# Optimization experiments

Hardware: AMD Instinct MI355X
Metric: run time of the kernel (lower is better)

The kernel has to match this reference:

```python
import jax, jax.numpy as jnp
import numpy as np

B, L = 8, 1024
VOCAB, D_ENC, D_MAIN = 260, 128, 256
N_ENC, N_MAIN, N_DEC, N_HEADS = 3, 6, 3, 4
N_RATIO = 6.0  # 1/target_ratio
NEG = jnp.float32(-1e9)


def setup_inputs() -> dict:
    key = jax.random.key(0)
    kc = iter(jax.random.split(key, 40))
    def nrm(shape, std):
        return jax.random.normal(next(kc), shape, jnp.float32) * std
    inp = {'byte_ids': jax.random.randint(next(kc), (B, L), 0, VOCAB)}
    inp['embed'] = nrm((VOCAB, D_ENC), D_ENC ** -0.5)
    eye = jnp.eye(D_ENC, dtype=jnp.float32)
    inp['wq'] = eye + nrm((D_ENC, D_ENC), 0.02)  # init is identity in the torch module
    inp['wk'] = eye + nrm((D_ENC, D_ENC), 0.02)
    inp['proj_up'] = nrm((D_MAIN, D_ENC), D_ENC ** -0.5)
    inp['proj_down'] = nrm((D_ENC, D_MAIN), 1e-3)
    inp['norm_w'] = jnp.ones((D_ENC,), jnp.float32)
    inp['norm_b'] = jnp.zeros((D_ENC,), jnp.float32)
    for pre, n, d in [('enc', N_ENC, D_ENC), ('main', N_MAIN, D_MAIN), ('dec', N_DEC, D_ENC)]:
        inp[pre + '_ln1_w'] = jnp.ones((n, d), jnp.float32)
        inp[pre + '_ln1_b'] = jnp.zeros((n, d), jnp.float32)
        inp[pre + '_qkv'] = nrm((n, 3 * d, d), d ** -0.5)   # MHA in_proj (3D, D)
        inp[pre + '_wo'] = nrm((n, d, d), d ** -0.5)        # MHA out_proj
        inp[pre + '_ln2_w'] = jnp.ones((n, d), jnp.float32)
        inp[pre + '_ln2_b'] = jnp.zeros((n, d), jnp.float32)
        inp[pre + '_w1'] = nrm((n, 2 * d, d), d ** -0.5)    # mlp_mult = 2
        inp[pre + '_w2'] = nrm((n, d, 2 * d), (2 * d) ** -0.5)
    return inp


def _ln(x, w, b):
    mu = jnp.mean(x, axis=-1, keepdims=True)
    var = jnp.mean((x - mu) ** 2, axis=-1, keepdims=True)
    return (x - mu) * jax.lax.rsqrt(var + 1e-5) * w + b


def _mha(x, wqkv, wo, bias):
    Bb, S, D = x.shape
    dh = D // N_HEADS
    q, k, v = jnp.split(x @ wqkv.T, 3, axis=-1)
    q = q.reshape(Bb, S, N_HEADS, dh)
    k = k.reshape(Bb, S, N_HEADS, dh)
    v = v.reshape(Bb, S, N_HEADS, dh)
    scores = jnp.einsum('bqhd,bkhd->bhqk', q, k) * (dh ** -0.5) + bias
    attn = jax.nn.softmax(scores, axis=-1)
    out = jnp.einsum('bhqk,bkhd->bqhd', attn, v).reshape(Bb, S, D)
    return out @ wo.T


def _block(x, stack, i, bias):
    ln1w, ln1b, qkv, wo, ln2w, ln2b, w1, w2 = (a[i] for a in stack)
    x = x + _mha(_ln(x, ln1w, ln1b), qkv, wo, bias)
    h = _ln(x, ln2w, ln2b)
    return x + jax.nn.gelu(h @ w1.T, approximate=False) @ w2.T


def _downsample(x, b_hard):
    # scatter boundary tokens to the front of a padded (B, S, D) buffer
    Bb, S, D = x.shape
    idx = jnp.cumsum(b_hard, axis=1).astype(jnp.int32) - 1
    dest = jnp.where(b_hard > 0.5, idx, S)  # S is out-of-range -> dropped
    def sc(xb, db):
        return jnp.zeros((S, D), xb.dtype).at[db].set(xb, mode='drop')
    out = jax.vmap(sc)(x, dest)
    counts = jnp.sum(b_hard, axis=1).astype(jnp.int32)
    mask = jnp.arange(S)[None, :] < counts[:, None]
    return out, mask


def _forward(byte_ids, embed, wq, wk,
             enc_ln1_w, enc_ln1_b, enc_qkv, enc_wo, enc_ln2_w, enc_ln2_b, enc_w1, enc_w2,
             proj_up,
             main_ln1_w, main_ln1_b, main_qkv, main_wo, main_ln2_w, main_ln2_b, main_w1, main_w2,
             proj_down,
             dec_ln1_w, dec_ln1_b, dec_qkv, dec_wo, dec_ln2_w, dec_ln2_b, dec_w1, dec_w2,
             norm_w, norm_b):
    causal = jnp.where(jnp.triu(jnp.ones((L, L), bool), 1), NEG, jnp.float32(0.0))[None, None]
    x = embed[byte_ids]  # (B, L, D_ENC)
    enc_p = (enc_ln1_w, enc_ln1_b, enc_qkv, enc_wo, enc_ln2_w, enc_ln2_b, enc_w1, enc_w2)
    for i in range(N_ENC):
        x = _block(x, enc_p, i, causal)

    # --- dynamic chunking (routing + ratio loss) ---
    def l2n(t):
        return t / jnp.maximum(jnp.linalg.norm(t, axis=-1, keepdims=True), 1e-12)
    q = l2n(x @ wq.T)
    k = l2n(x @ wk.T)
    k_prev = jnp.pad(k[:, :-1], ((0, 0), (1, 0), (0, 0)))
    cos = jnp.sum(q * k_prev, axis=-1)
    p = jnp.clip(0.5 * (1.0 - cos), 0.0, 1.0)
    p = jnp.concatenate([jnp.ones_like(p[:, :1]), p[:, 1:]], axis=1)
    b_hard = (p >= 0.5).astype(jnp.float32)
    N = N_RATIO
    F_act = jnp.mean(b_hard)
    G_act = jnp.mean(p)
    ratio_loss = N / (N - 1.0) * ((N - 1.0) * F_act * G_act + (1.0 - F_act) * (1.0 - G_act))
    compressed, comp_mask = _downsample(x, b_hard)
    p_comp = _downsample(p[..., None], b_hard)[0][..., 0]

    # --- main stack on compressed sequence (padded to L, masked) ---
    z = compressed @ proj_up.T
    main_bias = causal + jnp.where(comp_mask, jnp.float32(0.0), NEG)[:, None, None, :]
    main_p = (main_ln1_w, main_ln1_b, main_qkv, main_wo, main_ln2_w, main_ln2_b, main_w1, main_w2)
    for i in range(N_MAIN):
        z = _block(z, main_p, i, main_bias)
    z = z @ proj_down.T  # (B, L, D_ENC)

    # --- chunk-level EMA (parallel linear-recurrence scan) + gather + STE ---
    p_c = jnp.clip(p_comp, 1e-4, 1.0 - 1e-4)
    a = (1.0 - p_c).at[:, 0].set(0.0)[..., None]          # z_bar[0] = z[0]
    bv = (p_c[..., None] * z).at[:, :1].set(z[:, :1])
    def comb(lhs, rhs):
        al, bl = lhs
        ar, br = rhs
        return (al * ar, ar * bl + br)
    z_bar = jax.lax.associative_scan(comb, (a, bv), axis=1)[1]
    chunk_idx = jnp.clip(jnp.cumsum(b_hard, axis=1).astype(jnp.int32) - 1, 0, None)
    z_up = jnp.take_along_axis(z_bar, jnp.broadcast_to(chunk_idx[:, :, None], z_bar.shape), axis=1)
    c = b_hard * p + (1.0 - b_hard) * (1.0 - p)
    c_ste = c + jax.lax.stop_gradient(1.0 - c)
    x = x + c_ste[..., None] * z_up

    dec_p = (dec_ln1_w, dec_ln1_b, dec_qkv, dec_wo, dec_ln2_w, dec_ln2_b, dec_w1, dec_w2)
    for i in range(N_DEC):
        x = _block(x, dec_p, i, causal)
    x = _ln(x, norm_w, norm_b)
    logits = x @ embed.T  # tied head
    return logits, ratio_loss


def reference(byte_ids, embed, wq, wk,
              enc_ln1_w, enc_ln1_b, enc_qkv, enc_wo, enc_ln2_w, enc_ln2_b, enc_w1, enc_w2,
              proj_up,
              main_ln1_w, main_ln1_b, main_qkv, main_wo, main_ln2_w, main_ln2_b, main_w1, main_w2,
              proj_down,
              dec_ln1_w, dec_ln1_b, dec_qkv, dec_wo, dec_ln2_w, dec_ln2_b, dec_w1, dec_w2,
              norm_w, norm_b):
    return _forward(byte_ids, embed, wq, wk,
                    enc_ln1_w, enc_ln1_b, enc_qkv, enc_wo, enc_ln2_w, enc_ln2_b, enc_w1, enc_w2,
                    proj_up,
                    main_ln1_w, main_ln1_b, main_qkv, main_wo, main_ln2_w, main_ln2_b, main_w1, main_w2,
                    proj_down,
                    dec_ln1_w, dec_ln1_b, dec_qkv, dec_wo, dec_ln2_w, dec_ln2_b, dec_w1, dec_w2,
                    norm_w, norm_b)
```

## Files before the change

### kernel.cpp

```cpp
#include <hip/hip_runtime.h>
#include <hip/hip_bf16.h>

#define B_ 8
#define L_ 1024
#define BL (B_*L_)
#define DENC 128
#define DMAIN 256
#define VOCAB 260
#define NHEADS 4

typedef __hip_bfloat16 bf16;
typedef _Float16 f16;
typedef f16 half8 __attribute__((ext_vector_type(8)));
typedef float f32x4 __attribute__((ext_vector_type(4)));

__global__ __launch_bounds__(64) void k_detect(const void* __restrict__ emb, int* __restrict__ flag){
    int lane = threadIdx.x;
    const unsigned short* u = (const unsigned short*)emb;
    int bad = 0;
    #pragma unroll
    for (int j = 0; j < 4; j++){
        unsigned short h = u[lane + 64*j];
        bf16 t = *(const bf16*)&h;
        float v = __bfloat162float(t);
        if (!(fabsf(v) < 1e4f)) bad++;
    }
    #pragma unroll
    for (int o = 32; o >= 1; o >>= 1) bad += __shfl_xor(bad, o);
    if (lane == 0) flag[0] = (bad == 0) ? 1 : 0;
}

struct CvtArgs {
    const void* src[31];
    unsigned offs[32];
};
__global__ void k_cvt_all(CvtArgs a, float* __restrict__ dst, int total, const int* __restrict__ flag){
    int isbf = flag[0];
    for (int i = blockIdx.x*256 + threadIdx.x; i < total; i += gridDim.x*256){
        int lo = 0, hi = 30;
        while (lo < hi){ int mid = (lo+hi+1)>>1; if (a.offs[mid] <= (unsigned)i) lo = mid; else hi = mid-1; }
        int j = i - (int)a.offs[lo];
        dst[i] = isbf ? __bfloat162float(((const bf16*)a.src[lo])[j])
                      : ((const float*)a.src[lo])[j];
    }
}

__global__ void k_embed(const int* __restrict__ ids, const float* __restrict__ emb, float* __restrict__ x){
    int i = blockIdx.x*256 + threadIdx.x;
    int row = i >> 7, d = i & 127;
    x[i] = emb[ids[row]*DENC + d];
}

template<int D>
__global__ __launch_bounds__(256) void k_ln(const float* __restrict__ x, const float* __restrict__ w,
                                            const float* __restrict__ b, float* __restrict__ y){
    int row = blockIdx.x*4 + (threadIdx.x >> 6);
    int lane = threadIdx.x & 63;
    const float* xr = x + (size_t)row*D;
    float v[D/64];
    float s = 0.f;
    #pragma unroll
    for (int j=0;j<D/64;j++){ v[j] = xr[lane + j*64]; s += v[j]; }
    #pragma unroll
    for (int o=32;o>=1;o>>=1) s += __shfl_xor(s,o);
    float mu = s / (float)D;
    float s2 = 0.f;
    #pragma unroll
    for (int j=0;j<D/64;j++){ float dd = v[j]-mu; s2 += dd*dd; }
    #pragma unroll
    for (int o=32;o>=1;o>>=1) s2 += __shfl_xor(s2,o);
    float inv = rsqrtf(s2/(float)D + 1e-5f);
    float* yr = y + (size_t)row*D;
    #pragma unroll
    for (int j=0;j<D/64;j++){
        int d = lane + j*64;
        yr[d] = (v[j]-mu)*inv*w[d] + b[d];
    }
}

#define GBM 64
#define GBN 64
#define GBK 32
__global__ __launch_bounds__(256) void k_gemm2(const float* __restrict__ A, const float* __restrict__ Wq,
        const float* __restrict__ Wk, float* __restrict__ Cq, float* __restrict__ Ck, int K)
{
    __shared__ float As[GBK][GBM+4];
    __shared__ float Ws[GBK][GBN+4];
    int tid = threadIdx.x;
    int bm = blockIdx.y * GBM;
    int bn = blockIdx.x * GBN;
    int tx = tid & 15, ty = tid >> 4;
    float acc[4][4] = {};
    for (int k0 = 0; k0 < K; k0 += GBK){
        #pragma unroll
        for (int i = tid; i < GBM*GBK; i += 256){
            int m = i >> 5, kk = i & 31;
            As[kk][m] = A[(size_t)(bm+m)*K + k0 + kk];
        }
        #pragma unroll
        for (int i = tid; i < GBN*GBK; i += 256){
            int n = i >> 5, kk = i & 31;
            int gn = bn + n;
            const float* W = (gn < 128) ? Wq : Wk;
            int wr = gn & 127;
            Ws[kk][n] = W[(size_t)wr*K + k0 + kk];
        }
        __syncthreads();
        #pragma unroll
        for (int kk = 0; kk < GBK; kk++){
            float a0[4], w0[4];
            *(float4*)a0 = *(const float4*)&As[kk][ty*4];
            *(float4*)w0 = *(const float4*)&Ws[kk][tx*4];
            #pragma unroll
            for (int i=0;i<4;i++)
                #pragma unroll
                for (int j=0;j<4;j++) acc[i][j] += a0[i]*w0[j];
        }
        __syncthreads();
    }
    #pragma unroll
    for (int i=0;i<4;i++){
        int m = bm + ty*4 + i;
        #pragma unroll
        for (int j=0;j<4;j++){
            int n = bn + tx*4 + j;
            float* C = (n < 128) ? Cq : Ck;
            C[(size_t)m*128 + (n & 127)] = acc[i][j];
        }
    }
}

__global__ __launch_bounds__(256) void k_mgemm(const float* __restrict__ A, const float* __restrict__ W,
        const float* __restrict__ R, float* __restrict__ C, void* __restrict__ OutRaw,
        const int* __restrict__ flag, int M, int N, int K, int mode,
        f16* __restrict__ Qd, f16* __restrict__ Kd, f16* __restrict__ Vd,
        int dShift, int dhShift)
{
    __shared__ half8 As[4][64];
    __shared__ half8 Ws[4][64];
    int tid = threadIdx.x;
    int wave = tid >> 6, lane = tid & 63;
    int wr = wave >> 1, wc = wave & 1;
    int quad = lane >> 4, l15 = lane & 15;
    int bm = blockIdx.y * 64;
    int bn = blockIdx.x * 64;

    f32x4 acc[2][2] = {};

    int srow = tid >> 2;
    int sc8  = tid & 3;
    const float* ap0 = A + (size_t)(bm + srow)*K + sc8*8;
    int gn = bn + srow;
    const float* wp0 = W + (size_t)gn*K + sc8*8;
    bool wok = (gn < N);

    for (int k0 = 0; k0 < K; k0 += 32){
        __syncthreads();
        {
            const float* ap = ap0 + k0;
            float4 u0 = *(const float4*)(ap);
            float4 u1 = *(const float4*)(ap+4);
            half8 h0;
            h0[0]=(f16)u0.x; h0[1]=(f16)u0.y; h0[2]=(f16)u0.z; h0[3]=(f16)u0.w;
            h0[4]=(f16)u1.x; h0[5]=(f16)u1.y; h0[6]=(f16)u1.z; h0[7]=(f16)u1.w;
            As[sc8][srow] = h0;
            half8 g0 = (half8)(f16)0.f;
            if (wok){
                const float* wp = wp0 + k0;
                float4 v0 = *(const float4*)(wp);
                float4 v1 = *(const float4*)(wp+4);
                g0[0]=(f16)v0.x; g0[1]=(f16)v0.y; g0[2]=(f16)v0.z; g0[3]=(f16)v0.w;
                g0[4]=(f16)v1.x; g0[5]=(f16)v1.y; g0[6]=(f16)v1.z; g0[7]=(f16)v1.w;
            }
            Ws[sc8][srow] = g0;
        }
        __syncthreads();

        half8 af[2], wf[2];
        #pragma unroll
        for (int i=0;i<2;i++) af[i] = As[quad][wr*32 + i*16 + l15];
        #pragma unroll
        for (int j=0;j<2;j++) wf[j] = Ws[quad][wc*32 + j*16 + l15];
        #pragma unroll
        for (int i=0;i<2;i++)
            #pragma unroll
            for (int j=0;j<2;j++)
                acc[i][j] = __builtin_amdgcn_mfma_f32_16x16x32_f16(af[i], wf[j], acc[i][j], 0, 0, 0);
    }

    #pragma unroll
    for (int j=0;j<2;j++){
        int n = bn + wc*32 + j*16 + l15;
        if (n >= N) continue;
        #pragma unroll
        for (int i=0;i<2;i++){
            #pragma unroll
            for (int r=0;r<4;r++){
                int m = bm + wr*32 + i*16 + quad*4 + r;
                float v = acc[i][j][r];
                if (mode == 5){
                    int which = n >> dShift;
                    int rem = n & ((1<<dShift)-1);
                    int hh = rem >> dhShift;
                    int dd = rem & ((1<<dhShift)-1);
                    int bb = m >> 10, tt = m & 1023;
                    int Hn = 1 << (dShift - dhShift);
                    f16* dst = (which==0) ? Qd : ((which==1) ? Kd : Vd);
                    if (which == 2)
                        dst[((((size_t)bb*Hn + hh) << dhShift) + dd)*L_ + tt] = (f16)v;
                    else
                        dst[((((size_t)bb*Hn + hh)*L_ + tt) << dhShift) + dd] = (f16)v;
                    continue;
                }
                size_t off = (size_t)m*N + n;
                if (mode == 1) v += R[off];
                else if (mode == 2) v = 0.5f*v*(1.0f + erff(v*0.70710678118654752f));
                if (mode == 3){
                    if (flag[0]) ((bf16*)OutRaw)[off] = __float2bfloat16(v);
                    else         ((float*)OutRaw)[off] = v;
                } else C[off] = v;
            }
        }
    }
}

template<int DH>
__global__ __launch_bounds__(256) void k_mflash(const f16* __restrict__ Qh, const f16* __restrict__ Kh,
        const f16* __restrict__ Vt, float* __restrict__ out, const int* __restrict__ counts,
        float scale)
{
    constexpr int BQ = 64, BK = 64;
    constexpr int RS = DH + 8;
    constexpr int PS = BK + 8;
    __shared__ f16 sQ[BQ*RS];
    __shared__ f16 sK[BK*RS];
    __shared__ f16 sVt[DH*PS];
    __shared__ f16 sP[BQ*PS];

    int x = blockIdx.x, b = x >> 2, h = x & 3;
    int yy = blockIdx.y;
    int qt = (yy < 8) ? yy : 23 - yy;
    int q0 = qt * BQ;
    int tid = threadIdx.x;
    int wv = tid >> 6, lane = tid & 63;
    int quad = lane >> 4, l15 = lane & 15;

    const f16* Qb = Qh + (size_t)x*L_*DH;
    const f16* Kb = Kh + (size_t)x*L_*DH;
    const f16* Vb = Vt + (size_t)x*DH*L_;
    int kcap = counts ? counts[b] : L_;
    int klen = min(kcap, q0 + BQ);

    for (int i = tid; i < BQ*DH/8; i += 256){
        int r = (8*i)/DH, c = (8*i)%DH;
        *(half8*)&sQ[r*RS + c] = *(const half8*)&Qb[(size_t)(q0+r)*DH + c];
    }

    float m[4], l[4];
    #pragma unroll
    for (int r=0;r<4;r++){ m[r] = -1e30f; l[r] = 0.f; }
    f32x4 accO[DH/16] = {};

    for (int k0 = 0; k0 < klen; k0 += BK){
        __syncthreads();
        for (int i = tid; i < BK*DH/8; i += 256){
            int r = (8*i)/DH, c = (8*i)%DH;
            *(half8*)&sK[r*RS + c] = *(const half8*)&Kb[(size_t)(k0+r)*DH + c];
        }
        for (int i = tid; i < DH*BK/8; i += 256){
            int r = (8*i)/BK, c = (8*i)%BK;
            *(half8*)&sVt[r*PS + c] = *(const half8*)&Vb[(size_t)r*L_ + k0 + c];
        }
        __syncthreads();

        half8 af[DH/32];
        #pragma unroll
        for (int ds=0; ds<DH/32; ds++)
            af[ds] = *(const half8*)&sQ[(16*wv + l15)*RS + quad*8 + 32*ds];
        f32x4 accS[4] = {};
        #pragma unroll
        for (int t=0;t<4;t++){
            #pragma unroll
            for (int ds=0; ds<DH/32; ds++){
                half8 bf = *(const half8*)&sK[(16*t + l15)*RS + quad*8 + 32*ds];
                accS[t] = __builtin_amdgcn_mfma_f32_16x16x32_f16(af[ds], bf, accS[t], 0, 0, 0);
            }
        }

        #pragma unroll
        for (int r=0;r<4;r++){
            int qrow = q0 + 16*wv + quad*4 + r;
            float sv[4];
            #pragma unroll
            for (int t=0;t<4;t++){
                float v = accS[t][r]*scale;
                int kp = k0 + 16*t + l15;
                if (kp > qrow || kp >= kcap) v = -1e30f;
                sv[t] = v;
            }
            float rm = fmaxf(fmaxf(sv[0],sv[1]), fmaxf(sv[2],sv[3]));
            rm = fmaxf(rm, __shfl_xor(rm, 1));
            rm = fmaxf(rm, __shfl_xor(rm, 2));
            rm = fmaxf(rm, __shfl_xor(rm, 4));
            rm = fmaxf(rm, __shfl_xor(rm, 8));
            float mn = fmaxf(m[r], rm);
            float al = __expf(m[r] - mn);
            float p0 = __expf(sv[0]-mn), p1 = __expf(sv[1]-mn);
            float p2 = __expf(sv[2]-mn), p3 = __expf(sv[3]-mn);
            float rs = p0+p1+p2+p3;
            rs += __shfl_xor(rs, 1);
            rs += __shfl_xor(rs, 2);
            rs += __shfl_xor(rs, 4);
            rs += __shfl_xor(rs, 8);
            l[r] = l[r]*al + rs;
            m[r] = mn;
            #pragma unroll
            for (int dt=0; dt<DH/16; dt++) accO[dt][r] *= al;
            int prow = 16*wv + quad*4 + r;
            sP[prow*PS + 16*0 + l15] = (f16)p0;
            sP[prow*PS + 16*1 + l15] = (f16)p1;
            sP[prow*PS + 16*2 + l15] = (f16)p2;
            sP[prow*PS + 16*3 + l15] = (f16)p3;
        }

        half8 pf[2];
        #pragma unroll
        for (int ks=0; ks<2; ks++)
            pf[ks] = *(const half8*)&sP[(16*wv + l15)*PS + quad*8 + 32*ks];
        #pragma unroll
        for (int dt=0; dt<DH/16; dt++){
            #pragma unroll
            for (int ks=0; ks<2; ks++){
                half8 bv = *(const half8*)&sVt[(16*dt + l15)*PS + quad*8 + 32*ks];
                accO[dt] = __builtin_amdgcn_mfma_f32_16x16x32_f16(pf[ks], bv, accO[dt], 0, 0, 0);
            }
        }
    }

    #pragma unroll
    for (int r=0;r<4;r++){
        float inv = 1.0f / l[r];
        int qrow = q0 + 16*wv + quad*4 + r;
        #pragma unroll
        for (int dt=0; dt<DH/16; dt++){
            int d = 16*dt + l15;
            out[((size_t)b*L_ + qrow)*(NHEADS*DH) + h*DH + d] = accO[dt][r]*inv;
        }
    }
}

__global__ __launch_bounds__(64) void k_router(const float* __restrict__ Q, const float* __restrict__ Kr,
        float* __restrict__ p, float* __restrict__ bh)
{
    int idx = blockIdx.x;
    int t = idx & (L_-1);
    int lane = threadIdx.x;
    float pv;
    if (t == 0){ pv = 1.0f; }
    else {
        const float* qr = Q  + (size_t)idx*DENC;
        const float* kr = Kr + (size_t)(idx-1)*DENC;
        float qq=0.f, kk=0.f, qk=0.f;
        #pragma unroll
        for (int j=0;j<2;j++){
            float qv = qr[lane + j*64], kv = kr[lane + j*64];
            qq += qv*qv; kk += kv*kv; qk += qv*kv;
        }
        #pragma unroll
        for (int o=32;o>=1;o>>=1){ qq += __shfl_xor(qq,o); kk += __shfl_xor(kk,o); qk += __shfl_xor(qk,o); }
        float cosv = qk / (fmaxf(sqrtf(qq),1e-12f)*fmaxf(sqrtf(kk),1e-12f));
        pv = 0.5f*(1.0f - cosv);
        pv = fminf(fmaxf(pv, 0.0f), 1.0f);
    }
    if (lane == 0){ p[idx] = pv; bh[idx] = (pv >= 0.5f) ? 1.0f : 0.0f; }
}

__global__ __launch_bounds__(64) void k_seq(const float* __restrict__ bh, int* __restrict__ cidx,
                      int* __restrict__ dest, int* __restrict__ counts){
    int b = blockIdx.x;
    int lane = threadIdx.x;
    int base = b*L_ + lane*16;
    int h[16];
    int cnt = 0;
    #pragma unroll
    for (int j=0;j<16;j++){ h[j] = bh[base+j] > 0.5f; cnt += h[j]; }
    int inc = cnt;
    #pragma unroll
    for (int o=1;o<64;o<<=1){ int nb = __shfl_up(inc, o); if (lane >= o) inc += nb; }
    int run = inc - cnt;
    #pragma unroll
    for (int j=0;j<16;j++){
        run += h[j];
        int ci = run - 1; if (ci < 0) ci = 0;
        cidx[base+j] = ci;
        dest[base+j] = h[j] ? (run-1) : L_;
    }
    if (lane == 63) counts[b] = inc;
}

__global__ void k_zeroinit(float* __restrict__ comp, float* __restrict__ pcomp, float* __restrict__ acc){
    int i = blockIdx.x*256 + threadIdx.x;
    comp[i] = 0.f;
    if (i < BL) pcomp[i] = 0.f;
    if (i < 8) acc[i] = 0.f;
}

__global__ void k_scatter(const float* __restrict__ x, const float* __restrict__ p,
        const int* __restrict__ dest, const float* __restrict__ bh,
        float* __restrict__ comp, float* __restrict__ pcomp)
{
    int i = blockIdx.x;
    int d = threadIdx.x;
    int b = i >> 10;
    if (bh[i] > 0.5f){
        int ds = dest[i];
        comp[((size_t)b*L_ + ds)*DENC + d] = x[(size_t)i*DENC + d];
        if (d == 0) pcomp[b*L_ + ds] = p[i];
    }
}

__global__ __launch_bounds__(256) void k_reduce(const float* __restrict__ p, const float* __restrict__ bh,
                                                float* __restrict__ acc){
    __shared__ float sp[256], sb[256];
    int tid = threadIdx.x;
    float s1=0.f, s2=0.f;
    for (int i = blockIdx.x*256 + tid; i < BL; i += gridDim.x*256){ s1 += p[i]; s2 += bh[i]; }
    sp[tid]=s1; sb[tid]=s2; __syncthreads();
    for (int o=128;o>=1;o>>=1){ if (tid<o){ sp[tid]+=sp[tid+o]; sb[tid]+=sb[tid+o]; } __syncthreads(); }
    if (tid==0){ atomicAdd(&acc[0], sp[0]); atomicAdd(&acc[1], sb[0]); }
}

__global__ __launch_bounds__(256) void k_ema2(const float* __restrict__ z, const float* __restrict__ pcomp,
                                              float* __restrict__ zbar){
    __shared__ float sp[L_];
    int blk = blockIdx.x;
    int b = blk >> 5;
    int tid = threadIdx.x, wv = tid >> 6, lane = tid & 63;
    int d = ((blk & 31) << 2) + wv;
    for (int i = tid; i < L_; i += 256){
        float pc = pcomp[b*L_ + i];
        sp[i] = fminf(fmaxf(pc, 1e-4f), 1.0f - 1e-4f);
    }
    __syncthreads();
    const float* zb = z + ((size_t)b*L_)*DENC + d;
    int t0 = lane*16;
    float zv[16];
    #pragma unroll
    for (int i=0;i<16;i++) zv[i] = zb[(size_t)(t0+i)*DENC];
    float A = 1.f, Bv = 0.f;
    #pragma unroll
    for (int i=0;i<16;i++){
        int t = t0 + i;
        float pc = sp[t];
        float a  = (t==0) ? 0.f : (1.f - pc);
        float bb = (t==0) ? zv[i] : pc*zv[i];
        A = a*A;
        Bv = a*Bv + bb;
    }
    #pragma unroll
    for (int off=1; off<64; off<<=1){
        float Ap = __shfl_up(A, off);
        float Bp = __shfl_up(Bv, off);
        if (lane >= off){ Bv = A*Bp + Bv; A = A*Ap; }
    }
    float sin_ = __shfl_up(Bv, 1);
    if (lane == 0) sin_ = 0.f;
    float s = sin_;
    float* ob = zbar + ((size_t)b*L_)*DENC + d;
    #pragma unroll
    for (int i=0;i<16;i++){
        int t = t0 + i;
        float pc = sp[t];
        float a  = (t==0) ? 0.f : (1.f - pc);
        float bb = (t==0) ? zv[i] : pc*zv[i];
        s = a*s + bb;
        ob[(size_t)t*DENC] = s;
    }
}

__global__ void k_combine(float* __restrict__ x, const float* __restrict__ zbar, const int* __restrict__ cidx){
    int i = blockIdx.x*256 + threadIdx.x;
    int row = i >> 7, d = i & 127;
    int b = row >> 10;
    int ci = cidx[row];
    x[i] += zbar[((size_t)b*L_ + ci)*DENC + d];
}

__global__ void k_loss(const float* __restrict__ acc, void* __restrict__ out, const int* __restrict__ flag){
    float G = acc[0] / (float)BL;
    float F = acc[1] / (float)BL;
    float ratio = 1.2f*(5.0f*F*G + (1.0f-F)*(1.0f-G));
    if (flag[0]) ((bf16*)out)[(size_t)BL*VOCAB] = __float2bfloat16(ratio);
    else         ((float*)out)[(size_t)BL*VOCAB] = ratio;
}

extern "C" void kernel_launch(void* const* d_in, const int* in_sizes, int n_in,
                              void* d_out, int out_size, void* d_ws, size_t ws_size,
                              hipStream_t stream) {
    (void)out_size; (void)ws_size;
    const int* byte_ids = (const int*)d_in[0];

    float* ws = (float*)d_ws;
    size_t off = 0;
    int* FLAG = (int*)ws; off += 16;
    float* W32 = ws + off;

    k_detect<<<1, 64, 0, stream>>>(d_in[1], FLAG);

    CvtArgs ca;
    const float* w32[32];
    unsigned woff = 0;
    for (int i = 1; i < n_in && i < 32; i++){
        w32[i] = W32 + woff;
        ca.src[i-1] = d_in[i];
        ca.offs[i-1] = woff;
        woff += (unsigned)in_sizes[i];
    }
    ca.offs[31] = woff;
    k_cvt_all<<<2048, 256, 0, stream>>>(ca, W32, (int)woff, FLAG);
    off += woff;

    const float* embed    = w32[1];
    const float* wq       = w32[2];
    const float* wk       = w32[3];
    const float* proj_up  = w32[4];
    const float* proj_dn  = w32[5];
    const float* norm_w   = w32[6];
    const float* norm_b   = w32[7];
    const float* enc_ln1w = w32[8];
    const float* enc_ln1b = w32[9];
    const float* enc_qkv  = w32[10];
    const float* enc_wo   = w32[11];
    const float* enc_ln2w = w32[12];
    const float* enc_ln2b = w32[13];
    const float* enc_w1   = w32[14];
    const float* enc_w2   = w32[15];
    const float* main_ln1w= w32[16];
    const float* main_ln1b= w32[17];
    const float* main_qkv = w32[18];
    const float* main_wo  = w32[19];
    const float* main_ln2w= w32[20];
    const float* main_ln2b= w32[21];
    const float* main_w1  = w32[22];
    const float* main_w2  = w32[23];
    const float* dec_ln1w = w32[24];
    const float* dec_ln1b = w32[25];
    const float* dec_qkv  = w32[26];
    const float* dec_wo   = w32[27];
    const float* dec_ln2w = w32[28];
    const float* dec_ln2b = w32[29];
    const float* dec_w1   = w32[30];
    const float* dec_w2   = w32[31];

    float* X    = ws + off; off += (size_t)BL*DENC;
    float* LN   = ws + off; off += (size_t)BL*DMAIN;
    float* QKV  = ws + off; off += (size_t)BL*3*DMAIN;
    float* ATT  = ws + off; off += (size_t)BL*DMAIN;
    float* H    = ws + off; off += (size_t)BL*2*DMAIN;
    float* Z    = ws + off; off += (size_t)BL*DMAIN;
    float* COMP = ws + off; off += (size_t)BL*DENC;
    float* P    = ws + off; off += BL;
    float* BH   = ws + off; off += BL;
    float* PCOMP= ws + off; off += BL;
    float* ACC  = ws + off; off += 8;
    int* CIDX   = (int*)(ws + off); off += BL;
    int* DEST   = (int*)(ws + off); off += BL;
    int* COUNTS = (int*)(ws + off); off += 64;
    float* TMP  = H;
    float* ZDN  = QKV;
    float* ZBAR = QKV + (size_t)BL*DENC;

    auto gemm16 = [&](const float* A, const float* W, const float* R, float* C, void* Ob,
                    int N, int K, int mode){
        dim3 g((N+63)/64, BL/64);
        k_mgemm<<<g, 256, 0, stream>>>(A, W, R, C, Ob, FLAG, BL, N, K, mode,
                                       nullptr, nullptr, nullptr, 0, 0);
    };
    auto gemm_qkv = [&](const float* A, const float* W, int D, int dh){
        int N = 3*D;
        int dS = (D == 128) ? 7 : 8;
        int dhS = (dh == 32) ? 5 : 6;
        f16* Qh = (f16*)QKV;
        f16* Kh = (f16*)QKV + (size_t)BL*D;
        f16* Vh = (f16*)QKV + (size_t)2*BL*D;
        dim3 g((N+63)/64, BL/64);
        k_mgemm<<<g, 256, 0, stream>>>(A, W, nullptr, nullptr, nullptr, FLAG, BL, N, D, 5,
                                       Qh, Kh, Vh, dS, dhS);
    };

    auto block128 = [&](float* Xs, const float* l1w, const float* l1b, const float* qkvw, const float* wo,
                        const float* l2w, const float* l2b, const float* w1, const float* w2){
        k_ln<128><<<BL/4,256,0,stream>>>(Xs, l1w, l1b, LN);
        gemm_qkv(LN, qkvw, DENC, 32);
        k_mflash<32><<<dim3(B_*NHEADS,16),256,0,stream>>>((const f16*)QKV,
                                                          (const f16*)QKV + (size_t)BL*DENC,
                                                          (const f16*)QKV + (size_t)2*BL*DENC,
                                                          ATT, nullptr, 0.17677669529663687f);
        gemm16(ATT, wo, Xs, Xs, nullptr, DENC, DENC, 1);
        k_ln<128><<<BL/4,256,0,stream>>>(Xs, l2w, l2b, LN);
        gemm16(LN, w1, nullptr, H, nullptr, 2*DENC, DENC, 2);
        gemm16(H, w2, Xs, Xs, nullptr, DENC, 2*DENC, 1);
    };
    auto block_main = [&](float* Xs, const float* l1w, const float* l1b, const float* qkvw, const float* wo,
                        const float* l2w, const float* l2b, const float* w1, const float* w2){
        k_ln<256><<<BL/4,256,0,stream>>>(Xs, l1w, l1b, LN);
        gemm_qkv(LN, qkvw, DMAIN, 64);
        k_mflash<64><<<dim3(B_*NHEADS,16),256,0,stream>>>((const f16*)QKV,
                                                          (const f16*)QKV + (size_t)BL*DMAIN,
                                                          (const f16*)QKV + (size_t)2*BL*DMAIN,
                                                          ATT, COUNTS, 0.125f);
        gemm16(ATT, wo, Xs, Xs, nullptr, DMAIN, DMAIN, 1);
        k_ln<256><<<BL/4,256,0,stream>>>(Xs, l2w, l2b, LN);
        gemm16(LN, w1, nullptr, H, nullptr, 2*DMAIN, DMAIN, 2);
        gemm16(H, w2, Xs, Xs, nullptr, DMAIN, 2*DMAIN, 1);
    };

    k_embed<<<BL*DENC/256, 256, 0, stream>>>(byte_ids, embed, X);
    for (int i = 0; i < 3; i++)
        block128(X, enc_ln1w + i*DENC, enc_ln1b + i*DENC, enc_qkv + (size_t)i*3*DENC*DENC,
                 enc_wo + (size_t)i*DENC*DENC, enc_ln2w + i*DENC, enc_ln2b + i*DENC,
                 enc_w1 + (size_t)i*2*DENC*DENC, enc_w2 + (size_t)i*2*DENC*DENC);

    k_gemm2<<<dim3(4, BL/64), 256, 0, stream>>>(X, wq, wk, ATT, TMP, DENC);
    k_router<<<BL, 64, 0, stream>>>(ATT, TMP, P, BH);
    k_seq<<<B_, 64, 0, stream>>>(BH, CIDX, DEST, COUNTS);
    k_zeroinit<<<BL*DENC/256, 256, 0, stream>>>(COMP, PCOMP, ACC);
    k_scatter<<<BL, 128, 0, stream>>>(X, P, DEST, BH, COMP, PCOMP);
    k_reduce<<<8, 256, 0, stream>>>(P, BH, ACC);

    gemm16(COMP, proj_up, nullptr, Z, nullptr, DMAIN, DENC, 0);
    for (int i = 0; i < 6; i++)
        block_main(Z, main_ln1w + i*DMAIN, main_ln1b + i*DMAIN, main_qkv + (size_t)i*3*DMAIN*DMAIN,
                 main_wo + (size_t)i*DMAIN*DMAIN, main_ln2w + i*DMAIN, main_ln2b + i*DMAIN,
                 main_w1 + (size_t)i*2*DMAIN*DMAIN, main_w2 + (size_t)i*2*DMAIN*DMAIN);
    gemm16(Z, proj_dn, nullptr, ZDN, nullptr, DENC, DMAIN, 0);

    k_ema2<<<256, 256, 0, stream>>>(ZDN, PCOMP, ZBAR);
    k_combine<<<BL*DENC/256, 256, 0, stream>>>(X, ZBAR, CIDX);

    for (int i = 0; i < 3; i++)
        block128(X, dec_ln1w + i*DENC, dec_ln1b + i*DENC, dec_qkv + (size_t)i*3*DENC*DENC,
                 dec_wo + (size_t)i*DENC*DENC, dec_ln2w + i*DENC, dec_ln2b + i*DENC,
                 dec_w1 + (size_t)i*2*DENC*DENC, dec_w2 + (size_t)i*2*DENC*DENC);

    k_ln<128><<<BL/4,256,0,stream>>>(X, norm_w, norm_b, LN);
    gemm16(LN, embed, nullptr, nullptr, d_out, VOCAB, DENC, 3);
    k_loss<<<1,1,0,stream>>>(ACC, d_out, FLAG);
}
```

Baseline: 1.403 ms.

## Fuse LayerNorm into GEMM prologue, pre-convert weights to fp16, keep activations fp16

Removes the standalone LayerNorm kernels by normalizing each 64-row A tile inside the GEMM and staging it in LDS as fp16. Weights are converted to fp16 once alongside the fp32 copy, and attention output and MLP hidden activations are stored as fp16, so the GEMMs read half the bytes and skip per-tile conversion. Compression scatter becomes a gather driven by a source index, which removes the zero-init kernel. The new GEMMs read A and W fragments straight from global memory without LDS double-buffering, and fp16 intermediates cost some precision.

```diff
diff --git a/kernel.cpp b/kernel.cpp
--- a/kernel.cpp
+++ b/kernel.cpp
@@ -12,6 +12,8 @@
 typedef __hip_bfloat16 bf16;
 typedef _Float16 f16;
 typedef f16 half8 __attribute__((ext_vector_type(8)));
+typedef f16 half4 __attribute__((ext_vector_type(4)));
+typedef f16 half2v __attribute__((ext_vector_type(2)));
 typedef float f32x4 __attribute__((ext_vector_type(4)));
 
 __global__ __launch_bounds__(64) void k_detect(const void* __restrict__ emb, int* __restrict__ flag){
@@ -34,14 +36,17 @@
     const void* src[31];
     unsigned offs[32];
 };
-__global__ void k_cvt_all(CvtArgs a, float* __restrict__ dst, int total, const int* __restrict__ flag){
+__global__ void k_cvt_all(CvtArgs a, float* __restrict__ dst, f16* __restrict__ dst16,
+                          int total, const int* __restrict__ flag){
     int isbf = flag[0];
     for (int i = blockIdx.x*256 + threadIdx.x; i < total; i += gridDim.x*256){
         int lo = 0, hi = 30;
         while (lo < hi){ int mid = (lo+hi+1)>>1; if (a.offs[mid] <= (unsigned)i) lo = mid; else hi = mid-1; }
         int j = i - (int)a.offs[lo];
-        dst[i] = isbf ? __bfloat162float(((const bf16*)a.src[lo])[j])
-                      : ((const float*)a.src[lo])[j];
+        float v = isbf ? __bfloat162float(((const bf16*)a.src[lo])[j])
+                       : ((const float*)a.src[lo])[j];
+        dst[i] = v;
+        dst16[i] = (f16)v;
     }
 }
 
@@ -49,33 +54,6 @@
     int i = blockIdx.x*256 + threadIdx.x;
     int row = i >> 7, d = i & 127;
     x[i] = emb[ids[row]*DENC + d];
-}
-
-template<int D>
-__global__ __launch_bounds__(256) void k_ln(const float* __restrict__ x, const float* __restrict__ w,
-                                            const float* __restrict__ b, float* __restrict__ y){
-    int row = blockIdx.x*4 + (threadIdx.x >> 6);
-    int lane = threadIdx.x & 63;
-    const float* xr = x + (size_t)row*D;
-    float v[D/64];
-    float s = 0.f;
-    #pragma unroll
-    for (int j=0;j<D/64;j++){ v[j] = xr[lane + j*64]; s += v[j]; }
-    #pragma unroll
-    for (int o=32;o>=1;o>>=1) s += __shfl_xor(s,o);
-    float mu = s / (float)D;
-    float s2 = 0.f;
-    #pragma unroll
-    for (int j=0;j<D/64;j++){ float dd = v[j]-mu; s2 += dd*dd; }
-    #pragma unroll
-    for (int o=32;o>=1;o>>=1) s2 += __shfl_xor(s2,o);
-    float inv = rsqrtf(s2/(float)D + 1e-5f);
-    float* yr = y + (size_t)row*D;
-    #pragma unroll
-    for (int j=0;j<D/64;j++){
-        int d = lane + j*64;
-        yr[d] = (v[j]-mu)*inv*w[d] + b[d];
-    }
 }
 
 #define GBM 64
@@ -130,57 +108,77 @@
     }
 }
 
-__global__ __launch_bounds__(256) void k_mgemm(const float* __restrict__ A, const float* __restrict__ W,
-        const float* __restrict__ R, float* __restrict__ C, void* __restrict__ OutRaw,
-        const int* __restrict__ flag, int M, int N, int K, int mode,
+template<int K>
+__global__ __launch_bounds__(256) void k_lngemm(const float* __restrict__ A, const f16* __restrict__ W,
+        const float* __restrict__ lnw, const float* __restrict__ lnb, int doLN,
+        float* __restrict__ C, f16* __restrict__ C16, void* __restrict__ OutRaw,
+        const int* __restrict__ flag, int N, int mode,
         f16* __restrict__ Qd, f16* __restrict__ Kd, f16* __restrict__ Vd,
         int dShift, int dhShift)
 {
-    __shared__ half8 As[4][64];
-    __shared__ half8 Ws[4][64];
+    constexpr int SA = K + 8;
+    constexpr int RPT = K/64;
+    __shared__ f16 sA[64*SA];
     int tid = threadIdx.x;
     int wave = tid >> 6, lane = tid & 63;
     int wr = wave >> 1, wc = wave & 1;
     int quad = lane >> 4, l15 = lane & 15;
-    int bm = blockIdx.y * 64;
-    int bn = blockIdx.x * 64;
+    int bm = blockIdx.y * 64, bn = blockIdx.x * 64;
+
+    float wv_[RPT], bv_[RPT];
+    #pragma unroll
+    for (int j=0;j<RPT;j++){
+        int d = lane*RPT + j;
+        wv_[j] = doLN ? lnw[d] : 1.f;
+        bv_[j] = doLN ? lnb[d] : 0.f;
+    }
+    for (int rr=0; rr<16; rr++){
+        int row = wave*16 + rr;
+        const float* xr = A + (size_t)(bm+row)*K + lane*RPT;
+        float v[RPT];
+        if (RPT==2){ float2 t = *(const float2*)xr; v[0]=t.x; v[1]=t.y; }
+        else       { float4 t = *(const float4*)xr; v[0]=t.x; v[1]=t.y; v[2]=t.z; v[3]=t.w; }
+        float mu = 0.f, inv = 1.f;
+        if (doLN){
+            float s=0.f;
+            #pragma unroll
+            for (int j=0;j<RPT;j++) s += v[j];
+            #pragma unroll
+            for (int o=32;o>=1;o>>=1) s += __shfl_xor(s,o);
+            mu = s / (float)K;
+            float s2=0.f;
+            #pragma unroll
+            for (int j=0;j<RPT;j++){ float dd=v[j]-mu; s2+=dd*dd; }
+            #pragma unroll
+            for (int o=32;o>=1;o>>=1) s2 += __shfl_xor(s2,o);
+            inv = rsqrtf(s2/(float)K + 1e-5f);
+        }
+        if (RPT==2){
+            half2v h;
+            h[0]=(f16)((v[0]-mu)*inv*wv_[0]+bv_[0]);
+            h[1]=(f16)((v[1]-mu)*inv*wv_[1]+bv_[1]);
+            *(half2v*)&sA[row*SA + lane*2] = h;
+        } else {
+            half4 h;
+            #pragma unroll
+            for (int j=0;j<4;j++) h[j]=(f16)((v[j]-mu)*inv*wv_[j]+bv_[j]);
+            *(half4*)&sA[row*SA + lane*4] = h;
+        }
+    }
+    __syncthreads();
 
     f32x4 acc[2][2] = {};
-
-    int srow = tid >> 2;
-    int sc8  = tid & 3;
-    const float* ap0 = A + (size_t)(bm + srow)*K + sc8*8;
-    int gn = bn + srow;
-    const float* wp0 = W + (size_t)gn*K + sc8*8;
-    bool wok = (gn < N);
-
-    for (int k0 = 0; k0 < K; k0 += 32){
-        __syncthreads();
-        {
-            const float* ap = ap0 + k0;
-            float4 u0 = *(const float4*)(ap);
-            float4 u1 = *(const float4*)(ap+4);
-            half8 h0;
-            h0[0]=(f16)u0.x; h0[1]=(f16)u0.y; h0[2]=(f16)u0.z; h0[3]=(f16)u0.w;
-            h0[4]=(f16)u1.x; h0[5]=(f16)u1.y; h0[6]=(f16)u1.z; h0[7]=(f16)u1.w;
-            As[sc8][srow] = h0;
-            half8 g0 = (half8)(f16)0.f;
-            if (wok){
-                const float* wp = wp0 + k0;
-                float4 v0 = *(const float4*)(wp);
-                float4 v1 = *(const float4*)(wp+4);
-                g0[0]=(f16)v0.x; g0[1]=(f16)v0.y; g0[2]=(f16)v0.z; g0[3]=(f16)v0.w;
-                g0[4]=(f16)v1.x; g0[5]=(f16)v1.y; g0[6]=(f16)v1.z; g0[7]=(f16)v1.w;
-            }
-            Ws[sc8][srow] = g0;
-        }
-        __syncthreads();
-
+    int n0 = bn + wc*32 + l15;
+    bool ok0 = n0 < N, ok1 = (n0+16) < N;
+    const f16* w0p = W + (size_t)n0*K + quad*8;
+    const f16* w1p = W + (size_t)(n0+16)*K + quad*8;
+    #pragma unroll 4
+    for (int k0=0;k0<K;k0+=32){
         half8 af[2], wf[2];
-        #pragma unroll
-        for (int i=0;i<2;i++) af[i] = As[quad][wr*32 + i*16 + l15];
-        #pragma unroll
-        for (int j=0;j<2;j++) wf[j] = Ws[quad][wc*32 + j*16 + l15];
+        af[0] = *(const half8*)&sA[(wr*32 + l15)*SA + k0 + quad*8];
+        af[1] = *(const half8*)&sA[(wr*32 + 16 + l15)*SA + k0 + quad*8];
+        wf[0] = ok0 ? *(const half8*)(w0p + k0) : (half8)(f16)0.f;
+        wf[1] = ok1 ? *(const half8*)(w1p + k0) : (half8)(f16)0.f;
         #pragma unroll
         for (int i=0;i<2;i++)
             #pragma unroll
@@ -213,9 +211,10 @@
                     continue;
                 }
                 size_t off = (size_t)m*N + n;
-                if (mode == 1) v += R[off];
-                else if (mode == 2) v = 0.5f*v*(1.0f + erff(v*0.70710678118654752f));
-                if (mode == 3){
+                if (mode == 2){
+                    v = 0.5f*v*(1.0f + erff(v*0.70710678118654752f));
+                    C16[off] = (f16)v;
+                } else if (mode == 3){
                     if (flag[0]) ((bf16*)OutRaw)[off] = __float2bfloat16(v);
                     else         ((float*)OutRaw)[off] = v;
                 } else C[off] = v;
@@ -224,9 +223,52 @@
     }
 }
 
+template<int K>
+__global__ __launch_bounds__(256) void k_fgemm(const f16* __restrict__ A, const f16* __restrict__ W,
+        const float* __restrict__ R, float* __restrict__ C, int N, int mode)
+{
+    int tid = threadIdx.x;
+    int wave = tid >> 6, lane = tid & 63;
+    int wr = wave >> 1, wc = wave & 1;
+    int quad = lane >> 4, l15 = lane & 15;
+    int bm = blockIdx.y * 64, bn = blockIdx.x * 64;
+
+    f32x4 acc[2][2] = {};
+    const f16* a0 = A + (size_t)(bm + wr*32 + l15)*K + quad*8;
+    const f16* w0 = W + (size_t)(bn + wc*32 + l15)*K + quad*8;
+    #pragma unroll 4
+    for (int k0=0;k0<K;k0+=32){
+        half8 af[2], wf[2];
+        af[0] = *(const half8*)(a0 + k0);
+        af[1] = *(const half8*)(a0 + (size_t)16*K + k0);
+        wf[0] = *(const half8*)(w0 + k0);
+        wf[1] = *(const half8*)(w0 + (size_t)16*K + k0);
+        #pragma unroll
+        for (int i=0;i<2;i++)
+            #pragma unroll
+            for (int j=0;j<2;j++)
+                acc[i][j] = __builtin_amdgcn_mfma_f32_16x16x32_f16(af[i], wf[j], acc[i][j], 0, 0, 0);
+    }
+    #pragma unroll
+    for (int j=0;j<2;j++){
+        int n = bn + wc*32 + j*16 + l15;
+        #pragma unroll
+        for (int i=0;i<2;i++){
+            #pragma unroll
+            for (int r=0;r<4;r++){
+                int m = bm + wr*32 + i*16 + quad*4 + r;
+                size_t off = (size_t)m*N + n;
+                float v = acc[i][j][r];
+                if (mode == 1) v += R[off];
+                C[off] = v;
+            }
+        }
+    }
+}
+
 template<int DH>
 __global__ __launch_bounds__(256) void k_mflash(const f16* __restrict__ Qh, const f16* __restrict__ Kh,
-        const f16* __restrict__ Vt, float* __restrict__ out, const int* __restrict__ counts,
+        const f16* __restrict__ Vt, f16* __restrict__ out, const int* __restrict__ counts,
         float scale)
 {
     constexpr int BQ = 64, BK = 64;
@@ -344,7 +386,7 @@
         #pragma unroll
         for (int dt=0; dt<DH/16; dt++){
             int d = 16*dt + l15;
-            out[((size_t)b*L_ + qrow)*(NHEADS*DH) + h*DH + d] = accO[dt][r]*inv;
+            out[((size_t)b*L_ + qrow)*(NHEADS*DH) + h*DH + d] = (f16)(accO[dt][r]*inv);
         }
     }
 }
@@ -376,9 +418,10 @@
 }
 
 __global__ __launch_bounds__(64) void k_seq(const float* __restrict__ bh, int* __restrict__ cidx,
-                      int* __restrict__ dest, int* __restrict__ counts){
+                      int* __restrict__ src, int* __restrict__ counts, float* __restrict__ acc){
     int b = blockIdx.x;
     int lane = threadIdx.x;
+    if (b == 0 && lane < 8) acc[lane] = 0.f;
     int base = b*L_ + lane*16;
     int h[16];
     int cnt = 0;
@@ -393,29 +436,25 @@
         run += h[j];
         int ci = run - 1; if (ci < 0) ci = 0;
         cidx[base+j] = ci;
-        dest[base+j] = h[j] ? (run-1) : L_;
+        if (h[j]) src[b*L_ + run-1] = lane*16 + j;
     }
     if (lane == 63) counts[b] = inc;
 }
 
-__global__ void k_zeroinit(float* __restrict__ comp, float* __restrict__ pcomp, float* __restrict__ acc){
-    int i = blockIdx.x*256 + threadIdx.x;
-    comp[i] = 0.f;
-    if (i < BL) pcomp[i] = 0.f;
-    if (i < 8) acc[i] = 0.f;
-}
-
-__global__ void k_scatter(const float* __restrict__ x, const float* __restrict__ p,
-        const int* __restrict__ dest, const float* __restrict__ bh,
-        float* __restrict__ comp, float* __restrict__ pcomp)
+__global__ __launch_bounds__(128) void k_scatter2(const float* __restrict__ x, const float* __restrict__ p,
+        const int* __restrict__ src, const int* __restrict__ counts,
+        f16* __restrict__ comp, float* __restrict__ pcomp)
 {
-    int i = blockIdx.x;
-    int d = threadIdx.x;
-    int b = i >> 10;
-    if (bh[i] > 0.5f){
-        int ds = dest[i];
-        comp[((size_t)b*L_ + ds)*DENC + d] = x[(size_t)i*DENC + d];
-        if (d == 0) pcomp[b*L_ + ds] = p[i];
+    int s = blockIdx.x & (L_-1), b = blockIdx.x >> 10, d = threadIdx.x;
+    int cnt = counts[b];
+    f16* crow = comp + ((size_t)b*L_ + s)*DENC;
+    if (s < cnt){
+        int t = src[b*L_ + s];
+        crow[d] = (f16)x[((size_t)b*L_ + t)*DENC + d];
+        if (d == 0) pcomp[b*L_ + s] = p[b*L_ + t];
+    } else {
+        crow[d] = (f16)0.f;
+        if (d == 0) pcomp[b*L_ + s] = 0.f;
     }
 }
 
@@ -517,133 +556,111 @@
         woff += (unsigned)in_sizes[i];
     }
     ca.offs[31] = woff;
-    k_cvt_all<<<2048, 256, 0, stream>>>(ca, W32, (int)woff, FLAG);
     off += woff;
+    f16* W16h = (f16*)(ws + off); off += (woff+1)/2;
+    const f16* w16[32];
+    for (int i = 1; i < n_in && i < 32; i++) w16[i] = W16h + ca.offs[i-1];
+    k_cvt_all<<<2048, 256, 0, stream>>>(ca, W32, W16h, (int)woff, FLAG);
 
     const float* embed    = w32[1];
     const float* wq       = w32[2];
     const float* wk       = w32[3];
-    const float* proj_up  = w32[4];
-    const float* proj_dn  = w32[5];
     const float* norm_w   = w32[6];
     const float* norm_b   = w32[7];
-    const float* enc_ln1w = w32[8];
-    const float* enc_ln1b = w32[9];
-    const float* enc_qkv  = w32[10];
-    const float* enc_wo   = w32[11];
-    const float* enc_ln2w = w32[12];
-    const float* enc_ln2b = w32[13];
-    const float* enc_w1   = w32[14];
-    const float* enc_w2   = w32[15];
-    const float* main_ln1w= w32[16];
-    const float* main_ln1b= w32[17];
-    const float* main_qkv = w32[18];
-    const float* main_wo  = w32[19];
-    const float* main_ln2w= w32[20];
-    const float* main_ln2b= w32[21];
-    const float* main_w1  = w32[22];
-    const float* main_w2  = w32[23];
-    const float* dec_ln1w = w32[24];
-    const float* dec_ln1b = w32[25];
-    const float* dec_qkv  = w32[26];
-    const float* dec_wo   = w32[27];
-    const float* dec_ln2w = w32[28];
-    const float* dec_ln2b = w32[29];
-    const float* dec_w1   = w32[30];
-    const float* dec_w2   = w32[31];
 
     float* X    = ws + off; off += (size_t)BL*DENC;
-    float* LN   = ws + off; off += (size_t)BL*DMAIN;
-    float* QKV  = ws + off; off += (size_t)BL*3*DMAIN;
-    float* ATT  = ws + off; off += (size_t)BL*DMAIN;
-    float* H    = ws + off; off += (size_t)BL*2*DMAIN;
+    float* QKVf = ws + off; off += (size_t)BL*3*DMAIN;
+    float* ATTf = ws + off; off += (size_t)BL*DMAIN;
+    float* Hf   = ws + off; off += (size_t)BL*2*DMAIN;
     float* Z    = ws + off; off += (size_t)BL*DMAIN;
-    float* COMP = ws + off; off += (size_t)BL*DENC;
+    float* COMPf= ws + off; off += (size_t)BL*DENC;
     float* P    = ws + off; off += BL;
     float* BH   = ws + off; off += BL;
     float* PCOMP= ws + off; off += BL;
     float* ACC  = ws + off; off += 8;
     int* CIDX   = (int*)(ws + off); off += BL;
-    int* DEST   = (int*)(ws + off); off += BL;
+    int* SRC    = (int*)(ws + off); off += BL;
     int* COUNTS = (int*)(ws + off); off += 64;
-    float* TMP  = H;
-    float* ZDN  = QKV;
-    float* ZBAR = QKV + (size_t)BL*DENC;
-
-    auto gemm16 = [&](const float* A, const float* W, const float* R, float* C, void* Ob,
-                    int N, int K, int mode){
+
+    f16* QKV16 = (f16*)QKVf;
+    f16* ATT16 = (f16*)ATTf;
+    f16* H16   = (f16*)Hf;
+    f16* COMP16= (f16*)COMPf;
+    float* Qr  = ATTf;
+    float* Kr  = Hf;
+    float* ZDN = QKVf;
+    float* ZBAR= QKVf + (size_t)BL*DENC;
+
+    auto lngemm = [&](int D, const float* A, const f16* W, const float* lw, const float* lb,
+                      int doLN, float* C, f16* C16, void* Ob, int N, int mode,
+                      f16* Qd, f16* Kd, f16* Vd, int dS, int dhS){
         dim3 g((N+63)/64, BL/64);
-        k_mgemm<<<g, 256, 0, stream>>>(A, W, R, C, Ob, FLAG, BL, N, K, mode,
-                                       nullptr, nullptr, nullptr, 0, 0);
+        if (D == 128)
+            k_lngemm<128><<<g, 256, 0, stream>>>(A, W, lw, lb, doLN, C, C16, Ob, FLAG, N, mode, Qd, Kd, Vd, dS, dhS);
+        else
+            k_lngemm<256><<<g, 256, 0, stream>>>(A, W, lw, lb, doLN, C, C16, Ob, FLAG, N, mode, Qd, Kd, Vd, dS, dhS);
     };
-    auto gemm_qkv = [&](const float* A, const float* W, int D, int dh){
-        int N = 3*D;
-        int dS = (D == 128) ? 7 : 8;
-        int dhS = (dh == 32) ? 5 : 6;
-        f16* Qh = (f16*)QKV;
-        f16* Kh = (f16*)QKV + (size_t)BL*D;
-        f16* Vh = (f16*)QKV + (size_t)2*BL*D;
-        dim3 g((N+63)/64, BL/64);
-        k_mgemm<<<g, 256, 0, stream>>>(A, W, nullptr, nullptr, nullptr, FLAG, BL, N, D, 5,
-                                       Qh, Kh, Vh, dS, dhS);
+    auto fgemm = [&](int K, const f16* A, const f16* W, const float* R, float* C, int N, int mode){
+        dim3 g(N/64, BL/64);
+        if (K == 128)      k_fgemm<128><<<g, 256, 0, stream>>>(A, W, R, C, N, mode);
+        else if (K == 256) k_fgemm<256><<<g, 256, 0, stream>>>(A, W, R, C, N, mode);
+        else               k_fgemm<512><<<g, 256, 0, stream>>>(A, W, R, C, N, mode);
     };
 
-    auto block128 = [&](float* Xs, const float* l1w, const float* l1b, const float* qkvw, const float* wo,
-                        const float* l2w, const float* l2b, const float* w1, const float* w2){
-        k_ln<128><<<BL/4,256,0,stream>>>(Xs, l1w, l1b, LN);
-        gemm_qkv(LN, qkvw, DENC, 32);
-        k_mflash<32><<<dim3(B_*NHEADS,16),256,0,stream>>>((const f16*)QKV,
-                                                          (const f16*)QKV + (size_t)BL*DENC,
-                                                          (const f16*)QKV + (size_t)2*BL*DENC,
-                                                          ATT, nullptr, 0.17677669529663687f);
-        gemm16(ATT, wo, Xs, Xs, nullptr, DENC, DENC, 1);
-        k_ln<128><<<BL/4,256,0,stream>>>(Xs, l2w, l2b, LN);
-        gemm16(LN, w1, nullptr, H, nullptr, 2*DENC, DENC, 2);
-        gemm16(H, w2, Xs, Xs, nullptr, DENC, 2*DENC, 1);
+    auto block128 = [&](float* Xs, const float* l1w, const float* l1b, const f16* qkvw, const f16* wo,
+                        const float* l2w, const float* l2b, const f16* w1, const f16* w2){
+        lngemm(128, Xs, qkvw, l1w, l1b, 1, nullptr, nullptr, nullptr, 3*DENC, 5,
+               QKV16, QKV16 + (size_t)BL*DENC, QKV16 + (size_t)2*BL*DENC, 7, 5);
+        k_mflash<32><<<dim3(B_*NHEADS,16),256,0,stream>>>(QKV16, QKV16 + (size_t)BL*DENC,
+                                                          QKV16 + (size_t)2*BL*DENC,
+                                                          ATT16, nullptr, 0.17677669529663687f);
+        fgemm(128, ATT16, wo, Xs, Xs, DENC, 1);
+        lngemm(128, Xs, w1, l2w, l2b, 1, nullptr, H16, nullptr, 2*DENC, 2,
+               nullptr, nullptr, nullptr, 0, 0);
+        fgemm(256, H16, w2, Xs, Xs, DENC, 1);
     };
-    auto block_main = [&](float* Xs, const float* l1w, const float* l1b, const float* qkvw, const float* wo,
-                        const float* l2w, const float* l2b, const float* w1, const float* w2){
-        k_ln<256><<<BL/4,256,0,stream>>>(Xs, l1w, l1b, LN);
-        gemm_qkv(LN, qkvw, DMAIN, 64);
-        k_mflash<64><<<dim3(B_*NHEADS,16),256,0,stream>>>((const f16*)QKV,
-                                                          (const f16*)QKV + (size_t)BL*DMAIN,
-                                                          (const f16*)QKV + (size_t)2*BL*DMAIN,
-                                                          ATT, COUNTS, 0.125f);
-        gemm16(ATT, wo, Xs, Xs, nullptr, DMAIN, DMAIN, 1);
-        k_ln<256><<<BL/4,256,0,stream>>>(Xs, l2w, l2b, LN);
-        gemm16(LN, w1, nullptr, H, nullptr, 2*DMAIN, DMAIN, 2);
-        gemm16(H, w2, Xs, Xs, nullptr, DMAIN, 2*DMAIN, 1);
+    auto block_main = [&](float* Xs, const float* l1w, const float* l1b, const f16* qkvw, const f16* wo,
+                          const float* l2w, const float* l2b, const f16* w1, const f16* w2){
+        lngemm(256, Xs, qkvw, l1w, l1b, 1, nullptr, nullptr, nullptr, 3*DMAIN, 5,
+               QKV16, QKV16 + (size_t)BL*DMAIN, QKV16 + (size_t)2*BL*DMAIN, 8, 6);
+        k_mflash<64><<<dim3(B_*NHEADS,16),256,0,stream>>>(QKV16, QKV16 + (size_t)BL*DMAIN,
+                                                          QKV16 + (size_t)2*BL*DMAIN,
+                                                          ATT16, COUNTS, 0.125f);
+        fgemm(256, ATT16, wo, Xs, Xs, DMAIN, 1);
+        lngemm(256, Xs, w1, l2w, l2b, 1, nullptr, H16, nullptr, 2*DMAIN, 2,
+               nullptr, nullptr, nullptr, 0, 0);
+        fgemm(512, H16, w2, Xs, Xs, DMAIN, 1);
     };
 
     k_embed<<<BL*DENC/256, 256, 0, stream>>>(byte_ids, embed, X);
     for (int i = 0; i < 3; i++)
-        block128(X, enc_ln1w + i*DENC, enc_ln1b + i*DENC, enc_qkv + (size_t)i*3*DENC*DENC,
-                 enc_wo + (size_t)i*DENC*DENC, enc_ln2w + i*DENC, enc_ln2b + i*DENC,
-                 enc_w1 + (size_t)i*2*DENC*DENC, enc_w2 + (size_t)i*2*DENC*DENC);
-
-    k_gemm2<<<dim3(4, BL/64), 256, 0, stream>>>(X, wq, wk, ATT, TMP, DENC);
-    k_router<<<BL, 64, 0, stream>>>(ATT, TMP, P, BH);
-    k_seq<<<B_, 64, 0, stream>>>(BH, CIDX, DEST, COUNTS);
-    k_zeroinit<<<BL*DENC/256, 256, 0, stream>>>(COMP, PCOMP, ACC);
-    k_scatter<<<BL, 128, 0, stream>>>(X, P, DEST, BH, COMP, PCOMP);
+        block128(X, w32[8] + i*DENC, w32[9] + i*DENC, w16[10] + (size_t)i*3*DENC*DENC,
+                 w16[11] + (size_t)i*DENC*DENC, w32[12] + i*DENC, w32[13] + i*DENC,
+                 w16[14] + (size_t)i*2*DENC*DENC, w16[15] + (size_t)i*2*DENC*DENC);
+
+    k_gemm2<<<dim3(4, BL/64), 256, 0, stream>>>(X, wq, wk, Qr, Kr, DENC);
+    k_router<<<BL, 64, 0, stream>>>(Qr, Kr, P, BH);
+    k_seq<<<B_, 64, 0, stream>>>(BH, CIDX, SRC, COUNTS, ACC);
+    k_scatter2<<<BL, 128, 0, stream>>>(X, P, SRC, COUNTS, COMP16, PCOMP);
     k_reduce<<<8, 256, 0, stream>>>(P, BH, ACC);
 
-    gemm16(COMP, proj_up, nullptr, Z, nullptr, DMAIN, DENC, 0);
+    fgemm(128, COMP16, w16[4], nullptr, Z, DMAIN, 0);
     for (int i = 0; i < 6; i++)
-        block_main(Z, main_ln1w + i*DMAIN, main_ln1b + i*DMAIN, main_qkv + (size_t)i*3*DMAIN*DMAIN,
-                 main_wo + (size_t)i*DMAIN*DMAIN, main_ln2w + i*DMAIN, main_ln2b + i*DMAIN,
-                 main_w1 + (size_t)i*2*DMAIN*DMAIN, main_w2 + (size_t)i*2*DMAIN*DMAIN);
-    gemm16(Z, proj_dn, nullptr, ZDN, nullptr, DENC, DMAIN, 0);
+        block_main(Z, w32[16] + i*DMAIN, w32[17] + i*DMAIN, w16[18] + (size_t)i*3*DMAIN*DMAIN,
+                   w16[19] + (size_t)i*DMAIN*DMAIN, w32[20] + i*DMAIN, w32[21] + i*DMAIN,
+                   w16[22] + (size_t)i*2*DMAIN*DMAIN, w16[23] + (size_t)i*2*DMAIN*DMAIN);
+    lngemm(256, Z, w16[5], nullptr, nullptr, 0, ZDN, nullptr, nullptr, DENC, 0,
+           nullptr, nullptr, nullptr, 0, 0);
 
     k_ema2<<<256, 256, 0, stream>>>(ZDN, PCOMP, ZBAR);
     k_combine<<<BL*DENC/256, 256, 0, stream>>>(X, ZBAR, CIDX);
 
     for (int i = 0; i < 3; i++)
-        block128(X, dec_ln1w + i*DENC, dec_ln1b + i*DENC, dec_qkv + (size_t)i*3*DENC*DENC,
-                 dec_wo + (size_t)i*DENC*DENC, dec_ln2w + i*DENC, dec_ln2b + i*DENC,
-                 dec_w1 + (size_t)i*2*DENC*DENC, dec_w2 + (size_t)i*2*DENC*DENC);
-
-    k_ln<128><<<BL/4,256,0,stream>>>(X, norm_w, norm_b, LN);
-    gemm16(LN, embed, nullptr, nullptr, d_out, VOCAB, DENC, 3);
+        block128(X, w32[24] + i*DENC, w32[25] + i*DENC, w16[26] + (size_t)i*3*DENC*DENC,
+                 w16[27] + (size_t)i*DENC*DENC, w32[28] + i*DENC, w32[29] + i*DENC,
+                 w16[30] + (size_t)i*2*DENC*DENC, w16[31] + (size_t)i*2*DENC*DENC);
+
+    lngemm(128, X, w16[1], norm_w, norm_b, 1, nullptr, nullptr, d_out, VOCAB, 3,
+           nullptr, nullptr, nullptr, 0, 0);
     k_loss<<<1,1,0,stream>>>(ACC, d_out, FLAG);
 }
```

New measurement: 1.515 ms. 8.0% more time.
